# Kernel optimization log

Measured on AMD Instinct MI355X. Metric: run time of the kernel, lower is better.

Reference implementation:

```python
import jax, jax.numpy as jnp
import numpy as np

N_NODES = 50000
N_EDGES = 600000
D_FEAT = 128
HIDDEN = 128
OUT = 64


def sage_conv(x, src, dst, Wl, bl, Wr, n_nodes):
    # message = x[src] gathered per edge; mean-aggregated at dst
    msg = x[src]                                            # [E, d]
    agg = jax.ops.segment_sum(msg, dst, num_segments=n_nodes)   # [N, d]
    cnt = jax.ops.segment_sum(jnp.ones((src.shape[0],), x.dtype), dst,
                              num_segments=n_nodes)             # [N]
    mean = agg / jnp.maximum(cnt, 1.0)[:, None]
    # PyG SAGEConv: lin_l(mean_neighbors) + lin_r(x_root); only lin_l has bias
    return mean @ Wl + bl + x @ Wr


def setup_inputs() -> dict:
    key = jax.random.key(0)
    ks = jax.random.split(key, 7)
    x = jax.random.normal(ks[0], (N_NODES, D_FEAT), dtype=jnp.float32)
    edge_index = jax.random.randint(ks[1], (2, N_EDGES), 0, N_NODES, dtype=jnp.int64)
    s1 = 1.0 / np.sqrt(D_FEAT)
    s2 = 1.0 / np.sqrt(HIDDEN)
    W1l = jax.random.normal(ks[2], (D_FEAT, HIDDEN), dtype=jnp.float32) * s1
    b1l = jnp.zeros((HIDDEN,), dtype=jnp.float32)
    W1r = jax.random.normal(ks[3], (D_FEAT, HIDDEN), dtype=jnp.float32) * s1
    W2l = jax.random.normal(ks[4], (HIDDEN, OUT), dtype=jnp.float32) * s2
    b2l = jnp.zeros((OUT,), dtype=jnp.float32)
    W2r = jax.random.normal(ks[5], (HIDDEN, OUT), dtype=jnp.float32) * s2
    return {"x": x, "edge_index": edge_index, "W1l": W1l, "b1l": b1l,
            "W1r": W1r, "W2l": W2l, "b2l": b2l, "W2r": W2r}


def reference(x, edge_index, W1l, b1l, W1r, W2l, b2l, W2r):
    n = x.shape[0]
    src, dst = edge_index[0], edge_index[1]
    h = sage_conv(x, src, dst, W1l, b1l, W1r, n)
    h = jax.nn.relu(h)
    out = sage_conv(h, src, dst, W2l, b2l, W2r, n)
    return out
```

## Files before the change

kernel.cpp:

```cpp
#include <hip/hip_runtime.h>
#include <cstdint>
#include <cstddef>

#define D 128
#define O2 64
#define PAD 136
#define CAP 64

typedef __attribute__((ext_vector_type(8))) short bf16x8;
typedef __attribute__((ext_vector_type(4))) float f32x4;

__device__ inline unsigned short f2bf(float f) {
  union { float f; uint32_t u; } v; v.f = f;
  uint32_t r = v.u + 0x7FFF + ((v.u >> 16) & 1);
  return (unsigned short)(r >> 16);
}
__device__ inline float bf_lo(uint32_t w) {
  union { uint32_t u; float f; } v; v.u = w << 16; return v.f;
}
__device__ inline float bf_hi(uint32_t w) {
  union { uint32_t u; float f; } v; v.u = w & 0xFFFF0000u; return v.f;
}

__device__ __forceinline__ void acc8(float* a, uint4 v) {
  a[0]+=bf_lo(v.x); a[1]+=bf_hi(v.x);
  a[2]+=bf_lo(v.y); a[3]+=bf_hi(v.y);
  a[4]+=bf_lo(v.z); a[5]+=bf_hi(v.z);
  a[6]+=bf_lo(v.w); a[7]+=bf_hi(v.w);
}

__global__ __launch_bounds__(256) void prep_all(
    const int* __restrict__ src, const int* __restrict__ dst,
    int* __restrict__ deg, unsigned short* __restrict__ eidx, int n_edges,
    const float* __restrict__ x, const float* __restrict__ W1l,
    const float* __restrict__ W1r, const float* __restrict__ W2l,
    const float* __restrict__ W2r, unsigned short* __restrict__ xb,
    unsigned short* __restrict__ WT1, unsigned short* __restrict__ WT2,
    int n_nodes, int edge_blocks, int xb_blocks)
{
  int b = blockIdx.x;
  if (b < edge_blocks) {
    const int half = n_edges >> 1;
    int e = b * 256 + threadIdx.x;
    if (e < half) {
      int d0 = dst[e],        d1 = dst[e + half];
      int s0 = src[e],        s1 = src[e + half];
      int p0 = atomicAdd(&deg[d0], 1);
      int p1 = atomicAdd(&deg[d1], 1);
      if (p0 < CAP) eidx[(size_t)d0 * CAP + p0] = (unsigned short)s0;
      if (p1 < CAP) eidx[(size_t)d1 * CAP + p1] = (unsigned short)s1;
    }
  } else if (b < edge_blocks + xb_blocks) {
    int i = (b - edge_blocks) * 256 + threadIdx.x;
    if (i < n_nodes * 32) {
      int n = i >> 5, q = i & 31;
      float4 v = ((const float4*)x)[(size_t)n * 32 + q];
      unsigned long long o =
          (unsigned long long)f2bf(v.x)
        | ((unsigned long long)f2bf(v.y) << 16)
        | ((unsigned long long)f2bf(v.z) << 32)
        | ((unsigned long long)f2bf(v.w) << 48);
      *(unsigned long long*)(xb + (size_t)n * 128 + q * 4) = o;
    }
  } else {
    int t = (b - edge_blocks - xb_blocks) * 256 + threadIdx.x;
    if (t < 128 * 256) {
      int n = t >> 8, k = t & 255;
      float w = (k < 128) ? W1l[(size_t)k * 128 + n] : W1r[(size_t)(k - 128) * 128 + n];
      WT1[t] = f2bf(w);
    } else {
      int u = t - 128 * 256;
      if (u < 128 * 128) {
        int n = u >> 7, k = u & 127;
        float w = (n < 64) ? W2l[(size_t)k * 64 + n] : W2r[(size_t)k * 64 + (n - 64)];
        WT2[u] = f2bf(w);
      }
    }
  }
}

__global__ __launch_bounds__(64) void fused_g1l12(
    const unsigned short* __restrict__ xb, const unsigned short* __restrict__ eidx,
    const int* __restrict__ deg, const unsigned short* __restrict__ WT1,
    const unsigned short* __restrict__ WT2, const float* __restrict__ b1l,
    unsigned short* __restrict__ hl, float* __restrict__ outp, int n_nodes)
{
  __shared__ unsigned short sx[16 * PAD];
  const int lane = threadIdx.x;
  const int g = lane >> 2;
  const int c = lane & 3;
  const int c8 = c * 8;
  const int N0 = blockIdx.x * 16;
  const int n = N0 + g;

  float a[32];
  #pragma unroll
  for (int i = 0; i < 32; i++) a[i] = 0.f;
  int dg = 0;
  if (n < n_nodes) dg = deg[n];
  const int cnt = min(dg, CAP);
  const unsigned short* bucket = eidx + (size_t)n * CAP;
  int p = 0;
  for (; p + 4 <= cnt; p += 4) {
    uint2 bi = *(const uint2*)(bucket + p);
    int s0 = bi.x & 0xFFFF, s1 = bi.x >> 16;
    int s2 = bi.y & 0xFFFF, s3 = bi.y >> 16;
    const unsigned short* r0 = xb + (size_t)s0 * 128 + c8;
    const unsigned short* r1 = xb + (size_t)s1 * 128 + c8;
    const unsigned short* r2 = xb + (size_t)s2 * 128 + c8;
    const unsigned short* r3 = xb + (size_t)s3 * 128 + c8;
    uint4 v[16];
    #pragma unroll
    for (int k = 0; k < 4; k++) {
      v[k]      = *(const uint4*)(r0 + k * 32);
      v[4 + k]  = *(const uint4*)(r1 + k * 32);
      v[8 + k]  = *(const uint4*)(r2 + k * 32);
      v[12 + k] = *(const uint4*)(r3 + k * 32);
    }
    #pragma unroll
    for (int q = 0; q < 4; q++)
      #pragma unroll
      for (int k = 0; k < 4; k++)
        acc8(&a[k * 8], v[q * 4 + k]);
  }
  for (; p < cnt; p++) {
    const unsigned short* r = xb + (size_t)bucket[p] * 128 + c8;
    #pragma unroll
    for (int k = 0; k < 4; k++) acc8(&a[k * 8], *(const uint4*)(r + k * 32));
  }

  const float ic = (n < n_nodes) ? 1.0f / fmaxf((float)dg, 1.0f) : 0.f;
  #pragma unroll
  for (int k = 0; k < 4; k++) {
    uint4 o;
    o.x = ((uint32_t)f2bf(a[k*8+1]*ic) << 16) | f2bf(a[k*8+0]*ic);
    o.y = ((uint32_t)f2bf(a[k*8+3]*ic) << 16) | f2bf(a[k*8+2]*ic);
    o.z = ((uint32_t)f2bf(a[k*8+5]*ic) << 16) | f2bf(a[k*8+4]*ic);
    o.w = ((uint32_t)f2bf(a[k*8+7]*ic) << 16) | f2bf(a[k*8+6]*ic);
    *(uint4*)(sx + g * PAD + k * 32 + c8) = o;
  }
  __syncthreads();

  const int quad = lane >> 4, l15 = lane & 15;
  const int ra = min(N0 + l15, n_nodes - 1);

  bf16x8 af[8];
  #pragma unroll
  for (int s = 0; s < 4; s++) {
    af[s]     = *(const bf16x8*)(sx + l15 * PAD + quad * 8 + s * 32);
    af[s + 4] = *(const bf16x8*)(xb + (size_t)ra * 128 + quad * 8 + s * 32);
  }
  f32x4 acc[8];
  #pragma unroll
  for (int tt = 0; tt < 8; tt++) acc[tt] = (f32x4){0.f, 0.f, 0.f, 0.f};
  const unsigned short* b1 = WT1 + (size_t)l15 * 256 + quad * 8;
  #pragma unroll
  for (int tt = 0; tt < 8; tt++) {
    #pragma unroll
    for (int s = 0; s < 8; s++) {
      bf16x8 bw = *(const bf16x8*)(b1 + (size_t)tt * 16 * 256 + s * 32);
      acc[tt] = __builtin_amdgcn_mfma_f32_16x16x32_bf16(af[s], bw, acc[tt], 0, 0, 0);
    }
  }
  __syncthreads();

  #pragma unroll
  for (int tt = 0; tt < 8; tt++) {
    int col = tt * 16 + l15;
    float bias = b1l[col];
    #pragma unroll
    for (int r = 0; r < 4; r++)
      sx[(quad * 4 + r) * PAD + col] = f2bf(fmaxf(acc[tt][r] + bias, 0.f));
  }
  __syncthreads();

  bf16x8 af2[4];
  #pragma unroll
  for (int s = 0; s < 4; s++)
    af2[s] = *(const bf16x8*)(sx + l15 * PAD + quad * 8 + s * 32);
  f32x4 acc2[8];
  #pragma unroll
  for (int tt = 0; tt < 8; tt++) acc2[tt] = (f32x4){0.f, 0.f, 0.f, 0.f};
  const unsigned short* b2 = WT2 + (size_t)l15 * 128 + quad * 8;
  #pragma unroll
  for (int tt = 0; tt < 8; tt++) {
    #pragma unroll
    for (int s = 0; s < 4; s++) {
      bf16x8 bw = *(const bf16x8*)(b2 + (size_t)tt * 16 * 128 + s * 32);
      acc2[tt] = __builtin_amdgcn_mfma_f32_16x16x32_bf16(af2[s], bw, acc2[tt], 0, 0, 0);
    }
  }

  #pragma unroll
  for (int tt = 0; tt < 8; tt++) {
    int col = tt * 16 + l15;
    #pragma unroll
    for (int r = 0; r < 4; r++) {
      int row = N0 + quad * 4 + r;
      if (row < n_nodes) {
        if (tt < 4) hl[(size_t)row * 64 + col] = f2bf(acc2[tt][r]);
        else        outp[(size_t)row * 64 + (col - 64)] = acc2[tt][r];
      }
    }
  }
}

__global__ __launch_bounds__(256) void gather2_kernel(
    const unsigned short* __restrict__ hl, const unsigned short* __restrict__ eidx,
    const int* __restrict__ deg, const float* __restrict__ b2l,
    float* __restrict__ out, int n_nodes)
{
  const int j = threadIdx.x & 7;
  const int g = threadIdx.x >> 3;
  const int n = blockIdx.x * 32 + g;
  if (n >= n_nodes) return;
  const int dg = deg[n];
  const int cnt = min(dg, CAP);
  const unsigned short* bucket = eidx + (size_t)n * CAP;
  float a[8];
  #pragma unroll
  for (int i = 0; i < 8; i++) a[i] = 0.f;
  int p = 0;
  for (; p + 8 <= cnt; p += 8) {
    uint4 bi = *(const uint4*)(bucket + p);
    int s[8];
    s[0] = bi.x & 0xFFFF; s[1] = bi.x >> 16;
    s[2] = bi.y & 0xFFFF; s[3] = bi.y >> 16;
    s[4] = bi.z & 0xFFFF; s[5] = bi.z >> 16;
    s[6] = bi.w & 0xFFFF; s[7] = bi.w >> 16;
    uint4 v[8];
    #pragma unroll
    for (int q = 0; q < 8; q++)
      v[q] = *(const uint4*)(hl + (size_t)s[q] * 64 + j * 8);
    #pragma unroll
    for (int q = 0; q < 8; q++) acc8(a, v[q]);
  }
  for (; p + 4 <= cnt; p += 4) {
    uint2 bi = *(const uint2*)(bucket + p);
    int s[4];
    s[0] = bi.x & 0xFFFF; s[1] = bi.x >> 16;
    s[2] = bi.y & 0xFFFF; s[3] = bi.y >> 16;
    uint4 v[4];
    #pragma unroll
    for (int q = 0; q < 4; q++)
      v[q] = *(const uint4*)(hl + (size_t)s[q] * 64 + j * 8);
    #pragma unroll
    for (int q = 0; q < 4; q++) acc8(a, v[q]);
  }
  for (; p < cnt; p++) {
    uint4 vA = *(const uint4*)(hl + (size_t)bucket[p] * 64 + j * 8);
    acc8(a, vA);
  }
  const float ic = 1.0f / fmaxf((float)dg, 1.0f);
  float* o = out + (size_t)n * 64 + j * 8;
  const float* bb = b2l + j * 8;
  float4 p0 = *(const float4*)(o);
  float4 p1 = *(const float4*)(o + 4);
  p0.x += bb[0] + a[0] * ic; p0.y += bb[1] + a[1] * ic;
  p0.z += bb[2] + a[2] * ic; p0.w += bb[3] + a[3] * ic;
  p1.x += bb[4] + a[4] * ic; p1.y += bb[5] + a[5] * ic;
  p1.z += bb[6] + a[6] * ic; p1.w += bb[7] + a[7] * ic;
  *(float4*)(o) = p0;
  *(float4*)(o + 4) = p1;
}

extern "C" void kernel_launch(void* const* d_in, const int* in_sizes, int n_in,
                              void* d_out, int out_size, void* d_ws, size_t ws_size,
                              hipStream_t stream)
{
  const float* x   = (const float*)d_in[0];
  const int*   ei  = (const int*)d_in[1];
  const float* W1l = (const float*)d_in[2];
  const float* b1l = (const float*)d_in[3];
  const float* W1r = (const float*)d_in[4];
  const float* W2l = (const float*)d_in[5];
  const float* b2l = (const float*)d_in[6];
  const float* W2r = (const float*)d_in[7];
  float* out = (float*)d_out;

  const int n_nodes = in_sizes[0] / D;
  const int n_edges = in_sizes[1] / 2;
  const int* src = ei;
  const int* dst = ei + n_edges;

  char* ws = (char*)d_ws;
  auto align256 = [](size_t v) { return (v + 255) & ~(size_t)255; };
  const size_t szN = align256((size_t)n_nodes * 4);

  size_t o = 0;
  int* deg = (int*)(ws + o);  o += szN;
  unsigned short* eidx = (unsigned short*)(ws + o); o += align256((size_t)n_nodes * CAP * 2);
  unsigned short* WT1  = (unsigned short*)(ws + o); o += align256(128 * 256 * 2);
  unsigned short* WT2  = (unsigned short*)(ws + o); o += align256(128 * 128 * 2);
  unsigned short* xb   = (unsigned short*)(ws + o); o += align256((size_t)n_nodes * 128 * 2);
  unsigned short* hl   = (unsigned short*)(ws + o); o += align256((size_t)n_nodes * 64 * 2);

  hipMemsetAsync(deg, 0, szN, stream);

  const int half = n_edges >> 1;
  const int edge_blocks = (half + 255) / 256;
  const int xb_blocks = (n_nodes * 32 + 255) / 256;
  const int w_blocks  = (128 * 256 + 128 * 128 + 255) / 256;

  prep_all<<<edge_blocks + xb_blocks + w_blocks, 256, 0, stream>>>(
      src, dst, deg, eidx, n_edges,
      x, W1l, W1r, W2l, W2r, xb, WT1, WT2, n_nodes, edge_blocks, xb_blocks);

  fused_g1l12<<<(n_nodes + 15) / 16, 64, 0, stream>>>(
      xb, eidx, deg, WT1, WT2, b1l, hl, out, n_nodes);

  gather2_kernel<<<(n_nodes + 31) / 32, 256, 0, stream>>>(
      hl, eidx, deg, b2l, out, n_nodes);
}
```

Baseline: 196.8 us.

## Double-buffer neighbor gathers and split fused GEMM across two waves

The fused layer kernel grows from one wave to two per 16-node block. Each node's 128-wide gather is split over 8 lanes instead of 4, which halves the per-thread accumulator registers. The MFMA output columns are also split between the two waves, with a separate shared buffer for the hidden activations so one barrier can be dropped. Both gather loops now use a software-pipelined A/B double buffer that issues the next group of four row loads before accumulating the current group. This is meant to hide gather latency and raise occupancy, at the cost of more live load registers and some duplicated A-fragment loads across waves.

```diff
diff --git a/kernel.cpp b/kernel.cpp
--- a/kernel.cpp
+++ b/kernel.cpp
@@ -27,6 +27,34 @@
   a[2]+=bf_lo(v.y); a[3]+=bf_hi(v.y);
   a[4]+=bf_lo(v.z); a[5]+=bf_hi(v.z);
   a[6]+=bf_lo(v.w); a[7]+=bf_hi(v.w);
+}
+
+__device__ __forceinline__ void issue4x(const unsigned short* __restrict__ xb,
+                                        uint2 bi, int j8, uint4 v[8]) {
+  int s0 = bi.x & 0xFFFF, s1 = bi.x >> 16;
+  int s2 = bi.y & 0xFFFF, s3 = bi.y >> 16;
+  const unsigned short* r0 = xb + (size_t)s0 * 128 + j8;
+  const unsigned short* r1 = xb + (size_t)s1 * 128 + j8;
+  const unsigned short* r2 = xb + (size_t)s2 * 128 + j8;
+  const unsigned short* r3 = xb + (size_t)s3 * 128 + j8;
+  v[0] = *(const uint4*)r0;  v[1] = *(const uint4*)(r0 + 64);
+  v[2] = *(const uint4*)r1;  v[3] = *(const uint4*)(r1 + 64);
+  v[4] = *(const uint4*)r2;  v[5] = *(const uint4*)(r2 + 64);
+  v[6] = *(const uint4*)r3;  v[7] = *(const uint4*)(r3 + 64);
+}
+__device__ __forceinline__ void consume4x(const uint4 v[8], float* a) {
+  #pragma unroll
+  for (int q = 0; q < 4; q++) { acc8(a, v[q * 2]); acc8(a + 8, v[q * 2 + 1]); }
+}
+
+__device__ __forceinline__ void issue4h(const unsigned short* __restrict__ hl,
+                                        uint2 bi, int j8, uint4 v[4]) {
+  int s0 = bi.x & 0xFFFF, s1 = bi.x >> 16;
+  int s2 = bi.y & 0xFFFF, s3 = bi.y >> 16;
+  v[0] = *(const uint4*)(hl + (size_t)s0 * 64 + j8);
+  v[1] = *(const uint4*)(hl + (size_t)s1 * 64 + j8);
+  v[2] = *(const uint4*)(hl + (size_t)s2 * 64 + j8);
+  v[3] = *(const uint4*)(hl + (size_t)s3 * 64 + j8);
 }
 
 __global__ __launch_bounds__(256) void prep_all(
@@ -79,127 +107,124 @@
   }
 }
 
-__global__ __launch_bounds__(64) void fused_g1l12(
+__global__ __launch_bounds__(128, 4) void fused_g1l12(
     const unsigned short* __restrict__ xb, const unsigned short* __restrict__ eidx,
     const int* __restrict__ deg, const unsigned short* __restrict__ WT1,
     const unsigned short* __restrict__ WT2, const float* __restrict__ b1l,
     unsigned short* __restrict__ hl, float* __restrict__ outp, int n_nodes)
 {
-  __shared__ unsigned short sx[16 * PAD];
-  const int lane = threadIdx.x;
-  const int g = lane >> 2;
-  const int c = lane & 3;
-  const int c8 = c * 8;
+  __shared__ unsigned short sm[16 * PAD];
+  __shared__ unsigned short sh[16 * PAD];
+  const int tid = threadIdx.x;
+  const int g = tid >> 3;
+  const int j8 = (tid & 7) * 8;
   const int N0 = blockIdx.x * 16;
   const int n = N0 + g;
 
-  float a[32];
-  #pragma unroll
-  for (int i = 0; i < 32; i++) a[i] = 0.f;
-  int dg = 0;
-  if (n < n_nodes) dg = deg[n];
+  float a[16];
+  #pragma unroll
+  for (int i = 0; i < 16; i++) a[i] = 0.f;
+  int dg = (n < n_nodes) ? deg[n] : 0;
   const int cnt = min(dg, CAP);
   const unsigned short* bucket = eidx + (size_t)n * CAP;
-  int p = 0;
-  for (; p + 4 <= cnt; p += 4) {
-    uint2 bi = *(const uint2*)(bucket + p);
-    int s0 = bi.x & 0xFFFF, s1 = bi.x >> 16;
-    int s2 = bi.y & 0xFFFF, s3 = bi.y >> 16;
-    const unsigned short* r0 = xb + (size_t)s0 * 128 + c8;
-    const unsigned short* r1 = xb + (size_t)s1 * 128 + c8;
-    const unsigned short* r2 = xb + (size_t)s2 * 128 + c8;
-    const unsigned short* r3 = xb + (size_t)s3 * 128 + c8;
-    uint4 v[16];
-    #pragma unroll
-    for (int k = 0; k < 4; k++) {
-      v[k]      = *(const uint4*)(r0 + k * 32);
-      v[4 + k]  = *(const uint4*)(r1 + k * 32);
-      v[8 + k]  = *(const uint4*)(r2 + k * 32);
-      v[12 + k] = *(const uint4*)(r3 + k * 32);
-    }
-    #pragma unroll
-    for (int q = 0; q < 4; q++)
-      #pragma unroll
-      for (int k = 0; k < 4; k++)
-        acc8(&a[k * 8], v[q * 4 + k]);
-  }
-  for (; p < cnt; p++) {
-    const unsigned short* r = xb + (size_t)bucket[p] * 128 + c8;
-    #pragma unroll
-    for (int k = 0; k < 4; k++) acc8(&a[k * 8], *(const uint4*)(r + k * 32));
+
+  const int full = cnt >> 2;
+  uint4 vA[8], vB[8];
+  uint2 biA = {0, 0}, biB = {0, 0};
+  if (full > 0) biA = *(const uint2*)(bucket);
+  if (full > 1) biB = *(const uint2*)(bucket + 4);
+  if (full > 0) issue4x(xb, biA, j8, vA);
+  int i = 1;
+  for (; i + 1 < full; i += 2) {
+    issue4x(xb, biB, j8, vB);
+    biA = *(const uint2*)(bucket + (i + 1) * 4);
+    consume4x(vA, a);
+    issue4x(xb, biA, j8, vA);
+    if (i + 2 < full) biB = *(const uint2*)(bucket + (i + 2) * 4);
+    consume4x(vB, a);
+  }
+  if (i < full)        { issue4x(xb, biB, j8, vB); consume4x(vA, a); consume4x(vB, a); }
+  else if (full > 0)   { consume4x(vA, a); }
+  for (int p = full * 4; p < cnt; p++) {
+    const unsigned short* r = xb + (size_t)bucket[p] * 128 + j8;
+    acc8(a, *(const uint4*)r);
+    acc8(a + 8, *(const uint4*)(r + 64));
   }
 
   const float ic = (n < n_nodes) ? 1.0f / fmaxf((float)dg, 1.0f) : 0.f;
-  #pragma unroll
-  for (int k = 0; k < 4; k++) {
-    uint4 o;
-    o.x = ((uint32_t)f2bf(a[k*8+1]*ic) << 16) | f2bf(a[k*8+0]*ic);
-    o.y = ((uint32_t)f2bf(a[k*8+3]*ic) << 16) | f2bf(a[k*8+2]*ic);
-    o.z = ((uint32_t)f2bf(a[k*8+5]*ic) << 16) | f2bf(a[k*8+4]*ic);
-    o.w = ((uint32_t)f2bf(a[k*8+7]*ic) << 16) | f2bf(a[k*8+6]*ic);
-    *(uint4*)(sx + g * PAD + k * 32 + c8) = o;
+  {
+    uint4 o0, o1;
+    o0.x = ((uint32_t)f2bf(a[1]*ic) << 16) | f2bf(a[0]*ic);
+    o0.y = ((uint32_t)f2bf(a[3]*ic) << 16) | f2bf(a[2]*ic);
+    o0.z = ((uint32_t)f2bf(a[5]*ic) << 16) | f2bf(a[4]*ic);
+    o0.w = ((uint32_t)f2bf(a[7]*ic) << 16) | f2bf(a[6]*ic);
+    o1.x = ((uint32_t)f2bf(a[9]*ic) << 16) | f2bf(a[8]*ic);
+    o1.y = ((uint32_t)f2bf(a[11]*ic) << 16) | f2bf(a[10]*ic);
+    o1.z = ((uint32_t)f2bf(a[13]*ic) << 16) | f2bf(a[12]*ic);
+    o1.w = ((uint32_t)f2bf(a[15]*ic) << 16) | f2bf(a[14]*ic);
+    *(uint4*)(sm + g * PAD + j8) = o0;
+    *(uint4*)(sm + g * PAD + 64 + j8) = o1;
   }
   __syncthreads();
 
+  const int lane = tid & 63;
+  const int wv   = tid >> 6;
   const int quad = lane >> 4, l15 = lane & 15;
   const int ra = min(N0 + l15, n_nodes - 1);
 
   bf16x8 af[8];
   #pragma unroll
   for (int s = 0; s < 4; s++) {
-    af[s]     = *(const bf16x8*)(sx + l15 * PAD + quad * 8 + s * 32);
+    af[s]     = *(const bf16x8*)(sm + l15 * PAD + quad * 8 + s * 32);
     af[s + 4] = *(const bf16x8*)(xb + (size_t)ra * 128 + quad * 8 + s * 32);
   }
-  f32x4 acc[8];
-  #pragma unroll
-  for (int tt = 0; tt < 8; tt++) acc[tt] = (f32x4){0.f, 0.f, 0.f, 0.f};
-  const unsigned short* b1 = WT1 + (size_t)l15 * 256 + quad * 8;
-  #pragma unroll
-  for (int tt = 0; tt < 8; tt++) {
+  f32x4 acc[4];
+  #pragma unroll
+  for (int tt = 0; tt < 4; tt++) acc[tt] = (f32x4){0.f, 0.f, 0.f, 0.f};
+  const unsigned short* b1 = WT1 + (size_t)(wv * 4) * 16 * 256 + (size_t)l15 * 256 + quad * 8;
+  #pragma unroll
+  for (int tt = 0; tt < 4; tt++) {
     #pragma unroll
     for (int s = 0; s < 8; s++) {
       bf16x8 bw = *(const bf16x8*)(b1 + (size_t)tt * 16 * 256 + s * 32);
       acc[tt] = __builtin_amdgcn_mfma_f32_16x16x32_bf16(af[s], bw, acc[tt], 0, 0, 0);
     }
   }
+  #pragma unroll
+  for (int tt = 0; tt < 4; tt++) {
+    int col = (wv * 4 + tt) * 16 + l15;
+    float bias = b1l[col];
+    #pragma unroll
+    for (int r = 0; r < 4; r++)
+      sh[(quad * 4 + r) * PAD + col] = f2bf(fmaxf(acc[tt][r] + bias, 0.f));
+  }
   __syncthreads();
 
-  #pragma unroll
-  for (int tt = 0; tt < 8; tt++) {
-    int col = tt * 16 + l15;
-    float bias = b1l[col];
-    #pragma unroll
-    for (int r = 0; r < 4; r++)
-      sx[(quad * 4 + r) * PAD + col] = f2bf(fmaxf(acc[tt][r] + bias, 0.f));
-  }
-  __syncthreads();
-
   bf16x8 af2[4];
   #pragma unroll
   for (int s = 0; s < 4; s++)
-    af2[s] = *(const bf16x8*)(sx + l15 * PAD + quad * 8 + s * 32);
-  f32x4 acc2[8];
-  #pragma unroll
-  for (int tt = 0; tt < 8; tt++) acc2[tt] = (f32x4){0.f, 0.f, 0.f, 0.f};
-  const unsigned short* b2 = WT2 + (size_t)l15 * 128 + quad * 8;
-  #pragma unroll
-  for (int tt = 0; tt < 8; tt++) {
+    af2[s] = *(const bf16x8*)(sh + l15 * PAD + quad * 8 + s * 32);
+  f32x4 acc2[4];
+  #pragma unroll
+  for (int tt = 0; tt < 4; tt++) acc2[tt] = (f32x4){0.f, 0.f, 0.f, 0.f};
+  const unsigned short* b2 = WT2 + (size_t)(wv * 4) * 16 * 128 + (size_t)l15 * 128 + quad * 8;
+  #pragma unroll
+  for (int tt = 0; tt < 4; tt++) {
     #pragma unroll
     for (int s = 0; s < 4; s++) {
       bf16x8 bw = *(const bf16x8*)(b2 + (size_t)tt * 16 * 128 + s * 32);
       acc2[tt] = __builtin_amdgcn_mfma_f32_16x16x32_bf16(af2[s], bw, acc2[tt], 0, 0, 0);
     }
   }
-
-  #pragma unroll
-  for (int tt = 0; tt < 8; tt++) {
-    int col = tt * 16 + l15;
+  #pragma unroll
+  for (int tt = 0; tt < 4; tt++) {
+    int gcol = (wv * 4 + tt) * 16 + l15;
     #pragma unroll
     for (int r = 0; r < 4; r++) {
       int row = N0 + quad * 4 + r;
       if (row < n_nodes) {
-        if (tt < 4) hl[(size_t)row * 64 + col] = f2bf(acc2[tt][r]);
-        else        outp[(size_t)row * 64 + (col - 64)] = acc2[tt][r];
+        if (wv == 0) hl[(size_t)row * 64 + gcol] = f2bf(acc2[tt][r]);
+        else         outp[(size_t)row * 64 + (gcol - 64)] = acc2[tt][r];
       }
     }
   }
@@ -210,7 +235,7 @@
     const int* __restrict__ deg, const float* __restrict__ b2l,
     float* __restrict__ out, int n_nodes)
 {
-  const int j = threadIdx.x & 7;
+  const int j8 = (threadIdx.x & 7) * 8;
   const int g = threadIdx.x >> 3;
   const int n = blockIdx.x * 32 + g;
   if (n >= n_nodes) return;
@@ -220,40 +245,42 @@
   float a[8];
   #pragma unroll
   for (int i = 0; i < 8; i++) a[i] = 0.f;
-  int p = 0;
-  for (; p + 8 <= cnt; p += 8) {
-    uint4 bi = *(const uint4*)(bucket + p);
-    int s[8];
-    s[0] = bi.x & 0xFFFF; s[1] = bi.x >> 16;
-    s[2] = bi.y & 0xFFFF; s[3] = bi.y >> 16;
-    s[4] = bi.z & 0xFFFF; s[5] = bi.z >> 16;
-    s[6] = bi.w & 0xFFFF; s[7] = bi.w >> 16;
-    uint4 v[8];
-    #pragma unroll
-    for (int q = 0; q < 8; q++)
-      v[q] = *(const uint4*)(hl + (size_t)s[q] * 64 + j * 8);
-    #pragma unroll
-    for (int q = 0; q < 8; q++) acc8(a, v[q]);
-  }
-  for (; p + 4 <= cnt; p += 4) {
-    uint2 bi = *(const uint2*)(bucket + p);
-    int s[4];
-    s[0] = bi.x & 0xFFFF; s[1] = bi.x >> 16;
-    s[2] = bi.y & 0xFFFF; s[3] = bi.y >> 16;
-    uint4 v[4];
-    #pragma unroll
-    for (int q = 0; q < 4; q++)
-      v[q] = *(const uint4*)(hl + (size_t)s[q] * 64 + j * 8);
-    #pragma unroll
-    for (int q = 0; q < 4; q++) acc8(a, v[q]);
-  }
-  for (; p < cnt; p++) {
-    uint4 vA = *(const uint4*)(hl + (size_t)bucket[p] * 64 + j * 8);
-    acc8(a, vA);
-  }
+
+  const int full = cnt >> 2;
+  uint4 vA[4], vB[4];
+  uint2 biA = {0, 0}, biB = {0, 0};
+  if (full > 0) biA = *(const uint2*)(bucket);
+  if (full > 1) biB = *(const uint2*)(bucket + 4);
+  if (full > 0) issue4h(hl, biA, j8, vA);
+  int i = 1;
+  for (; i + 1 < full; i += 2) {
+    issue4h(hl, biB, j8, vB);
+    biA = *(const uint2*)(bucket + (i + 1) * 4);
+    #pragma unroll
+    for (int q = 0; q < 4; q++) acc8(a, vA[q]);
+    issue4h(hl, biA, j8, vA);
+    if (i + 2 < full) biB = *(const uint2*)(bucket + (i + 2) * 4);
+    #pragma unroll
+    for (int q = 0; q < 4; q++) acc8(a, vB[q]);
+  }
+  if (i < full) {
+    issue4h(hl, biB, j8, vB);
+    #pragma unroll
+    for (int q = 0; q < 4; q++) acc8(a, vA[q]);
+    #pragma unroll
+    for (int q = 0; q < 4; q++) acc8(a, vB[q]);
+  } else if (full > 0) {
+    #pragma unroll
+    for (int q = 0; q < 4; q++) acc8(a, vA[q]);
+  }
+  for (int p = full * 4; p < cnt; p++) {
+    uint4 vT = *(const uint4*)(hl + (size_t)bucket[p] * 64 + j8);
+    acc8(a, vT);
+  }
+
   const float ic = 1.0f / fmaxf((float)dg, 1.0f);
-  float* o = out + (size_t)n * 64 + j * 8;
-  const float* bb = b2l + j * 8;
+  float* o = out + (size_t)n * 64 + j8;
+  const float* bb = b2l + j8;
   float4 p0 = *(const float4*)(o);
   float4 p1 = *(const float4*)(o + 4);
   p0.x += bb[0] + a[0] * ic; p0.y += bb[1] + a[1] * ic;
@@ -306,7 +333,7 @@
       src, dst, deg, eidx, n_edges,
       x, W1l, W1r, W2l, W2r, xb, WT1, WT2, n_nodes, edge_blocks, xb_blocks);
 
-  fused_g1l12<<<(n_nodes + 15) / 16, 64, 0, stream>>>(
+  fused_g1l12<<<(n_nodes + 15) / 16, 128, 0, stream>>>(
       xb, eidx, deg, WT1, WT2, b1l, hl, out, n_nodes);
 
   gather2_kernel<<<(n_nodes + 31) / 32, 256, 0, stream>>>(
```

Measured after the change: 238.6 us. 1.21x slower.
